# Kernel optimization log

Measured on AMD Instinct MI355X. Metric: run time of the kernel, lower is better.

The kernel has to match this reference:

```python
import jax, jax.numpy as jnp
import numpy as np

B, T, C, IMG = 16, 1024, 4, 64
HID_C = 16                 # self.c (hidden_dim before *image_size)
H = HID_C * IMG            # 1024 GRU hidden size
IN = C * IMG               # 256 GRU input size
L = 2                      # num_layers


def setup_inputs() -> dict:
    key = jax.random.key(0)
    ks = jax.random.split(key, 10)
    s_in = 1.0 / np.sqrt(H)
    return {
        "x": jax.random.normal(ks[0], (B, T, C, IMG), jnp.float32),
        "h0": jnp.zeros((L, B, H), jnp.float32),
        "w_ih_0": jax.random.normal(ks[1], (3 * H, IN), jnp.float32) * s_in,
        "w_hh_0": jax.random.normal(ks[2], (3 * H, H), jnp.float32) * s_in,
        "b_ih_0": jax.random.normal(ks[3], (3 * H,), jnp.float32) * s_in,
        "b_hh_0": jax.random.normal(ks[4], (3 * H,), jnp.float32) * s_in,
        "w_ih_1": jax.random.normal(ks[5], (3 * H, H), jnp.float32) * s_in,
        "w_hh_1": jax.random.normal(ks[6], (3 * H, H), jnp.float32) * s_in,
        "b_ih_1": jax.random.normal(ks[7], (3 * H,), jnp.float32) * s_in,
        "b_hh_1": jax.random.normal(ks[8], (3 * H,), jnp.float32) * s_in,
    }


def _gru_layer(xs, h0, w_ih, w_hh, b_ih, b_hh):
    # xs: [b,t,in], h0: [b,H]. Precompute input-gate matmuls over all t.
    gx = jnp.einsum("bti,gi->btg", xs, w_ih) + b_ih  # [b,t,3H]

    def step(hprev, gx_t):
        gh = hprev @ w_hh.T + b_hh                   # [b,3H]
        xr, xz, xn = jnp.split(gx_t, 3, axis=-1)
        hr, hz, hn = jnp.split(gh, 3, axis=-1)
        r = jax.nn.sigmoid(xr + hr)
        z = jax.nn.sigmoid(xz + hz)
        n = jnp.tanh(xn + r * hn)
        hnew = (1.0 - z) * n + z * hprev
        return hnew, hnew

    h_last, ys = jax.lax.scan(step, h0, jnp.swapaxes(gx, 0, 1))
    return jnp.swapaxes(ys, 0, 1), h_last            # [b,t,H], [b,H]


def reference(x, h0, w_ih_0, w_hh_0, b_ih_0, b_hh_0,
              w_ih_1, w_hh_1, b_ih_1, b_hh_1):
    b, t, c, h = x.shape
    xs = x.reshape(b, t, c * h)
    y0, h_last0 = _gru_layer(xs, h0[0], w_ih_0, w_hh_0, b_ih_0, b_hh_0)
    y1, h_last1 = _gru_layer(y0, h0[1], w_ih_1, w_hh_1, b_ih_1, b_hh_1)
    y = y1.reshape(b, t, HID_C, h)
    last_states = jnp.stack([h_last0, h_last1], axis=0)  # [L,b,H]
    return y, last_states
```

## Files before the change

### kernel.cpp

```cpp
#include <hip/hip_runtime.h>
#include <stdint.h>

#define T_ 1024

typedef float  floatx4 __attribute__((ext_vector_type(4)));
typedef short  shortx8 __attribute__((ext_vector_type(8)));
typedef unsigned long long u64;

union U16 { u64 q[2]; unsigned d[4]; shortx8 v; };

__device__ __forceinline__ unsigned short f2bf(float f) {
  union { float f; unsigned u; } v; v.f = f;
  return (unsigned short)((v.u + 0x7FFFu + ((v.u >> 16) & 1u)) >> 16);
}
__device__ __forceinline__ unsigned pkbf(float lo, float hi) {
  unsigned r;
  asm("v_cvt_pk_bf16_f32 %0, %1, %2" : "=v"(r) : "v"(lo), "v"(hi));
  return r;
}
__device__ __forceinline__ u64 lda(const u64* p) {
  return __hip_atomic_load(p, __ATOMIC_RELAXED, __HIP_MEMORY_SCOPE_AGENT);
}
__device__ __forceinline__ void sta(u64* p, u64 v) {
  __hip_atomic_store(p, v, __ATOMIC_RELAXED, __HIP_MEMORY_SCOPE_AGENT);
}

__global__ void prep_kernel(uint4* __restrict__ fz) {
  long gid = (long)blockIdx.x * 256 + threadIdx.x;
  if (gid < 786432L) { uint4 z; z.x = z.y = z.z = z.w = 0u; fz[gid] = z; }
}

#define MFMA __builtin_amdgcn_mfma_f32_16x16x32_bf16

template<int L>
__device__ __forceinline__ void gru_wave(int lb, int tid,
    const float* __restrict__ x,
    const float* __restrict__ whh, const float* __restrict__ wih,
    const float* __restrict__ bih, const float* __restrict__ bhh,
    u64* __restrict__ y0buf, u64* __restrict__ h1ring,
    u64* __restrict__ f0, u64* __restrict__ f1,
    float* __restrict__ dout,
    short* __restrict__ wlds, float (*part)[4][4][16][17])
{
  constexpr int KW  = L ? 2048 : 1280;
  constexpr int WS  = KW + 8;
  constexpr int NC  = L ? 8 : 16;
  constexpr int NR  = 3 * NC;
  constexpr int KXs = L ? 1024 : 256;
  const int cb = lb * NC;
  const int w  = tid >> 6;
  const int l  = tid & 63;
  const int lr = l & 15, lq = l >> 4;
  const int c  = L ? (lr & 7) : lr;

  for (int i = tid; i < NR * (KW / 8); i += 256) {
    int row = i / (KW / 8);
    int k   = (i % (KW / 8)) * 8;
    int g = row / NC, cc = row % NC;
    const float* src = (k < 1024) ? (whh + (long)(g * 1024 + cb + cc) * 1024 + k)
                                  : (wih + (long)(g * 1024 + cb + cc) * KXs + (k - 1024));
    float4 a = *(const float4*)src;
    float4 b = *(const float4*)(src + 4);
    uint4 t4;
    t4.x = pkbf(a.x, a.y); t4.y = pkbf(a.z, a.w);
    t4.z = pkbf(b.x, b.y); t4.w = pkbf(b.z, b.w);
    *(uint4*)(wlds + row * WS + k) = t4;
  }

  const int gb = tid >> (L ? 3 : 4);
  const int gc = tid & (NC - 1);
  const bool isg = tid < 16 * NC;
  float bir = 0, biz = 0, bin = 0, bhr = 0, bhz = 0, bhn = 0;
  if (isg) {
    bir = bih[cb + gc];        bhr = bhh[cb + gc];
    biz = bih[1024 + cb + gc]; bhz = bhh[1024 + cb + gc];
    bin = bih[2048 + cb + gc]; bhn = bhh[2048 + cb + gc];
  }
  __syncthreads();

  const short* w0 = wlds + (0 * NC + c) * WS;
  const short* w1 = wlds + (1 * NC + c) * WS;
  const short* w2 = wlds + (2 * NC + c) * WS;

  float hp = 0.f;

  for (int t = 0; t < T_; ++t) {
    floatx4 ar = {0.f, 0.f, 0.f, 0.f};
    floatx4 az = ar, anh = ar, anx = ar;

    if constexpr (L == 0) {
#pragma unroll
      for (int j = 0; j < 2; ++j) {
        const int kt = w * 2 + j;
        const float* xs = x + (long)lr * 262144 + (long)t * 256 + kt * 32 + lq * 8;
        float4 a = *(const float4*)xs;
        float4 b = *(const float4*)(xs + 4);
        U16 u;
        u.d[0] = pkbf(a.x, a.y); u.d[1] = pkbf(a.z, a.w);
        u.d[2] = pkbf(b.x, b.y); u.d[3] = pkbf(b.z, b.w);
        const int ko = 1024 + kt * 32 + lq * 8;
        ar  = MFMA(u.v, *(const shortx8*)(w0 + ko), ar,  0, 0, 0);
        az  = MFMA(u.v, *(const shortx8*)(w1 + ko), az,  0, 0, 0);
        anx = MFMA(u.v, *(const shortx8*)(w2 + ko), anx, 0, 0, 0);
      }
      if (t > 0) {
        const u64* fp = f0 + ((long)(t - 1) * 64 + (w * 16 + lr)) * 8 + lq;
        for (;;) {
          u64 fl = lda(fp);
          if (__all(fl != 0)) break;
          __builtin_amdgcn_s_sleep(1);
        }
        const u64* base = y0buf + ((long)(t - 1) * 16 + lr) * 256 + w * 64 + lq * 2;
        u64 q[16];
#pragma unroll
        for (int j = 0; j < 8; ++j) {
          q[2 * j]     = lda(base + j * 8);
          q[2 * j + 1] = lda(base + j * 8 + 1);
        }
#pragma unroll
        for (int j = 0; j < 8; ++j) {
          U16 u; u.q[0] = q[2 * j]; u.q[1] = q[2 * j + 1];
          const int ko = (w * 8 + j) * 32 + lq * 8;
          ar  = MFMA(u.v, *(const shortx8*)(w0 + ko), ar,  0, 0, 0);
          az  = MFMA(u.v, *(const shortx8*)(w1 + ko), az,  0, 0, 0);
          anh = MFMA(u.v, *(const shortx8*)(w2 + ko), anh, 0, 0, 0);
        }
      }
    } else {
      const u64* fpy = f0 + ((long)t * 64 + (w * 16 + lr)) * 8 + lq;
      const u64* fph = f1 + ((long)(t > 0 ? t - 1 : 0) * 128 + (w * 32 + (l & 31))) * 8 + (l >> 5);
      for (;;) {
        u64 fy = lda(fpy);
        u64 fh = (t > 0) ? lda(fph) : 1ull;
        if (__all(fy != 0 && fh != 0)) break;
        __builtin_amdgcn_s_sleep(1);
      }
      const u64* yb = y0buf + ((long)t * 16 + lr) * 256 + w * 64 + lq * 2;
      u64 qy[16], qh[16];
#pragma unroll
      for (int j = 0; j < 8; ++j) {
        qy[2 * j]     = lda(yb + j * 8);
        qy[2 * j + 1] = lda(yb + j * 8 + 1);
      }
      if (t > 0) {
        const u64* hb = h1ring + ((long)((t - 1) & 7) * 16 + lr) * 256 + w * 64 + lq * 2;
#pragma unroll
        for (int j = 0; j < 8; ++j) {
          qh[2 * j]     = lda(hb + j * 8);
          qh[2 * j + 1] = lda(hb + j * 8 + 1);
        }
      }
#pragma unroll
      for (int j = 0; j < 8; ++j) {
        U16 u; u.q[0] = qy[2 * j]; u.q[1] = qy[2 * j + 1];
        const int ko = 1024 + (w * 8 + j) * 32 + lq * 8;
        ar  = MFMA(u.v, *(const shortx8*)(w0 + ko), ar,  0, 0, 0);
        az  = MFMA(u.v, *(const shortx8*)(w1 + ko), az,  0, 0, 0);
        anx = MFMA(u.v, *(const shortx8*)(w2 + ko), anx, 0, 0, 0);
      }
      if (t > 0) {
#pragma unroll
        for (int j = 0; j < 8; ++j) {
          U16 u; u.q[0] = qh[2 * j]; u.q[1] = qh[2 * j + 1];
          const int ko = (w * 8 + j) * 32 + lq * 8;
          ar  = MFMA(u.v, *(const shortx8*)(w0 + ko), ar,  0, 0, 0);
          az  = MFMA(u.v, *(const shortx8*)(w1 + ko), az,  0, 0, 0);
          anh = MFMA(u.v, *(const shortx8*)(w2 + ko), anh, 0, 0, 0);
        }
      }
    }

    const int par = t & 1;
    if (L == 0 || lr < 8) {
#pragma unroll
      for (int r4 = 0; r4 < 4; ++r4) {
        const int b = lq * 4 + r4;
        part[par][w][0][b][lr] = ar[r4];
        part[par][w][1][b][lr] = az[r4];
        part[par][w][2][b][lr] = anh[r4];
        part[par][w][3][b][lr] = anx[r4];
      }
    }
    __syncthreads();

    if (isg) {
      float sr = 0, sz = 0, snh = 0, snx = 0;
#pragma unroll
      for (int ww = 0; ww < 4; ++ww) {
        sr  += part[par][ww][0][gb][gc];
        sz  += part[par][ww][1][gb][gc];
        snh += part[par][ww][2][gb][gc];
        snx += part[par][ww][3][gb][gc];
      }
      float r = 1.f / (1.f + __expf(-(sr + bir + bhr)));
      float z = 1.f / (1.f + __expf(-(sz + biz + bhz)));
      float targ = snx + bin + r * (snh + bhn);
      float e2 = __expf(2.f * targ);
      float n = 1.f - 2.f / (e2 + 1.f);
      float hn = (1.f - z) * n + z * hp;
      hp = hn;

      unsigned hv = f2bf(hn);
      unsigned v1 = (unsigned)__shfl_down((int)hv, 1);
      unsigned v2 = (unsigned)__shfl_down((int)hv, 2);
      unsigned v3 = (unsigned)__shfl_down((int)hv, 3);

      if constexpr (L == 0) {
        if ((gc & 3) == 0) {
          u64 word = (u64)(hv | (v1 << 16)) | ((u64)(v2 | (v3 << 16)) << 32);
          sta(y0buf + ((long)t * 16 + gb) * 256 + ((cb + gc) >> 2), word);
        }
        asm volatile("s_waitcnt vmcnt(0)" ::: "memory");
        if (l == 0)
          sta(f0 + ((long)t * 64 + lb) * 8 + w, 1ull);
        if (t == T_ - 1)
          dout[16777216L + (long)gb * 1024 + cb + gc] = hn;
      } else {
        if ((gc & 3) == 0) {
          u64 word = (u64)(hv | (v1 << 16)) | ((u64)(v2 | (v3 << 16)) << 32);
          sta(h1ring + ((long)(t & 7) * 16 + gb) * 256 + ((cb + gc) >> 2), word);
        }
        asm volatile("s_waitcnt vmcnt(0)" ::: "memory");
        if (l == 0)
          sta(f1 + ((long)t * 128 + lb) * 8 + w, 1ull);
        unsigned fv = __float_as_uint(hn);
        unsigned fw2 = (unsigned)__shfl_down((int)fv, 1);
        if ((gc & 1) == 0)
          *(u64*)(dout + (long)gb * 1048576 + (long)t * 1024 + cb + gc) =
              (u64)fv | ((u64)fw2 << 32);
        if (t == T_ - 1)
          dout[16777216L + 16384 + (long)gb * 1024 + cb + gc] = hn;
      }
    }
  }
}

__global__ __launch_bounds__(256, 1) void gru_kernel(
    const float* __restrict__ x,
    const float* __restrict__ whh0, const float* __restrict__ wih0,
    const float* __restrict__ bih0, const float* __restrict__ bhh0,
    const float* __restrict__ whh1, const float* __restrict__ wih1,
    const float* __restrict__ bih1, const float* __restrict__ bhh1,
    u64* y0buf, u64* h1ring, u64* f0, u64* f1, float* dout)
{
  __shared__ __align__(16) short wlds[48 * 1288];
  __shared__ float part[2][4][4][16][17];
  const int bid = blockIdx.x, tid = threadIdx.x;
  if (bid < 64)
    gru_wave<0>(bid, tid, x, whh0, wih0, bih0, bhh0, y0buf, h1ring, f0, f1, dout, wlds, part);
  else
    gru_wave<1>(bid - 64, tid, x, whh1, wih1, bih1, bhh1, y0buf, h1ring, f0, f1, dout, wlds, part);
}

extern "C" void kernel_launch(void* const* d_in, const int* in_sizes, int n_in,
                              void* d_out, int out_size, void* d_ws, size_t ws_size,
                              hipStream_t stream) {
  (void)in_sizes; (void)n_in; (void)out_size; (void)ws_size;
  const float* x    = (const float*)d_in[0];
  const float* wih0 = (const float*)d_in[2];
  const float* whh0 = (const float*)d_in[3];
  const float* bih0 = (const float*)d_in[4];
  const float* bhh0 = (const float*)d_in[5];
  const float* wih1 = (const float*)d_in[6];
  const float* whh1 = (const float*)d_in[7];
  const float* bih1 = (const float*)d_in[8];
  const float* bhh1 = (const float*)d_in[9];
  char* ws = (char*)d_ws;
  u64* y0buf  = (u64*)(ws + 0L);
  u64* h1ring = (u64*)(ws + 33554432L);
  u64* f0     = (u64*)(ws + 33816576L);
  u64* f1     = (u64*)(ws + 38010880L);
  float* out  = (float*)d_out;

  prep_kernel<<<3072, 256, 0, stream>>>((uint4*)f0);
  gru_kernel<<<192, 256, 0, stream>>>(x, whh0, wih0, bih0, bhh0,
                                      whh1, wih1, bih1, bhh1,
                                      y0buf, h1ring, f0, f1, out);
}
```

Baseline: 6.362 ms.

## Use one flag per block instead of per-wave flags for cross-block step signaling

```diff
diff --git a/kernel.cpp b/kernel.cpp
--- a/kernel.cpp
+++ b/kernel.cpp
@@ -27,7 +27,7 @@
 
 __global__ void prep_kernel(uint4* __restrict__ fz) {
   long gid = (long)blockIdx.x * 256 + threadIdx.x;
-  if (gid < 786432L) { uint4 z; z.x = z.y = z.z = z.w = 0u; fz[gid] = z; }
+  if (gid < 98304L) { uint4 z; z.x = z.y = z.z = z.w = 0u; fz[gid] = z; }
 }
 
 #define MFMA __builtin_amdgcn_mfma_f32_16x16x32_bf16
@@ -104,7 +104,7 @@
         anx = MFMA(u.v, *(const shortx8*)(w2 + ko), anx, 0, 0, 0);
       }
       if (t > 0) {
-        const u64* fp = f0 + ((long)(t - 1) * 64 + (w * 16 + lr)) * 8 + lq;
+        const u64* fp = f0 + (long)(t - 1) * 64 + l;
         for (;;) {
           u64 fl = lda(fp);
           if (__all(fl != 0)) break;
@@ -127,13 +127,13 @@
         }
       }
     } else {
-      const u64* fpy = f0 + ((long)t * 64 + (w * 16 + lr)) * 8 + lq;
-      const u64* fph = f1 + ((long)(t > 0 ? t - 1 : 0) * 128 + (w * 32 + (l & 31))) * 8 + (l >> 5);
-      for (;;) {
-        u64 fy = lda(fpy);
-        u64 fh = (t > 0) ? lda(fph) : 1ull;
-        if (__all(fy != 0 && fh != 0)) break;
-        __builtin_amdgcn_s_sleep(1);
+      {
+        const u64* fy = f0 + (long)t * 64 + l;
+        for (;;) {
+          u64 fl = lda(fy);
+          if (__all(fl != 0)) break;
+          __builtin_amdgcn_s_sleep(1);
+        }
       }
       const u64* yb = y0buf + ((long)t * 16 + lr) * 256 + w * 64 + lq * 2;
       u64 qy[16], qh[16];
@@ -143,6 +143,12 @@
         qy[2 * j + 1] = lda(yb + j * 8 + 1);
       }
       if (t > 0) {
+        const u64* fh = f1 + (long)(t - 1) * 128 + l;
+        for (;;) {
+          u64 a = lda(fh), b = lda(fh + 64);
+          if (__all(a != 0 && b != 0)) break;
+          __builtin_amdgcn_s_sleep(1);
+        }
         const u64* hb = h1ring + ((long)((t - 1) & 7) * 16 + lr) * 256 + w * 64 + lq * 2;
 #pragma unroll
         for (int j = 0; j < 8; ++j) {
@@ -183,6 +189,7 @@
     }
     __syncthreads();
 
+    float hn = 0.f;
     if (isg) {
       float sr = 0, sz = 0, snh = 0, snx = 0;
 #pragma unroll
@@ -197,39 +204,39 @@
       float targ = snx + bin + r * (snh + bhn);
       float e2 = __expf(2.f * targ);
       float n = 1.f - 2.f / (e2 + 1.f);
-      float hn = (1.f - z) * n + z * hp;
+      hn = (1.f - z) * n + z * hp;
       hp = hn;
 
       unsigned hv = f2bf(hn);
       unsigned v1 = (unsigned)__shfl_down((int)hv, 1);
       unsigned v2 = (unsigned)__shfl_down((int)hv, 2);
       unsigned v3 = (unsigned)__shfl_down((int)hv, 3);
-
-      if constexpr (L == 0) {
-        if ((gc & 3) == 0) {
-          u64 word = (u64)(hv | (v1 << 16)) | ((u64)(v2 | (v3 << 16)) << 32);
+      if ((gc & 3) == 0) {
+        u64 word = (u64)(hv | (v1 << 16)) | ((u64)(v2 | (v3 << 16)) << 32);
+        if constexpr (L == 0)
           sta(y0buf + ((long)t * 16 + gb) * 256 + ((cb + gc) >> 2), word);
-        }
-        asm volatile("s_waitcnt vmcnt(0)" ::: "memory");
-        if (l == 0)
-          sta(f0 + ((long)t * 64 + lb) * 8 + w, 1ull);
+        else
+          sta(h1ring + ((long)(t & 7) * 16 + gb) * 256 + ((cb + gc) >> 2), word);
+      }
+    }
+
+    asm volatile("s_waitcnt vmcnt(0)" ::: "memory");
+    __syncthreads();
+    if (tid == 0)
+      sta((L ? f1 + (long)t * 128 : f0 + (long)t * 64) + lb, 1ull);
+
+    if (isg) {
+      if constexpr (L == 1) {
+        unsigned fv = __float_as_uint(hn);
+        unsigned f2v = (unsigned)__shfl_down((int)fv, 1);
+        if ((gc & 1) == 0)
+          *(u64*)(dout + (long)gb * 1048576 + (long)t * 1024 + cb + gc) =
+              (u64)fv | ((u64)f2v << 32);
+        if (t == T_ - 1)
+          dout[16777216L + 16384 + (long)gb * 1024 + cb + gc] = hn;
+      } else {
         if (t == T_ - 1)
           dout[16777216L + (long)gb * 1024 + cb + gc] = hn;
-      } else {
-        if ((gc & 3) == 0) {
-          u64 word = (u64)(hv | (v1 << 16)) | ((u64)(v2 | (v3 << 16)) << 32);
-          sta(h1ring + ((long)(t & 7) * 16 + gb) * 256 + ((cb + gc) >> 2), word);
-        }
-        asm volatile("s_waitcnt vmcnt(0)" ::: "memory");
-        if (l == 0)
-          sta(f1 + ((long)t * 128 + lb) * 8 + w, 1ull);
-        unsigned fv = __float_as_uint(hn);
-        unsigned fw2 = (unsigned)__shfl_down((int)fv, 1);
-        if ((gc & 1) == 0)
-          *(u64*)(dout + (long)gb * 1048576 + (long)t * 1024 + cb + gc) =
-              (u64)fv | ((u64)fw2 << 32);
-        if (t == T_ - 1)
-          dout[16777216L + 16384 + (long)gb * 1024 + cb + gc] = hn;
       }
     }
   }
@@ -269,10 +276,10 @@
   u64* y0buf  = (u64*)(ws + 0L);
   u64* h1ring = (u64*)(ws + 33554432L);
   u64* f0     = (u64*)(ws + 33816576L);
-  u64* f1     = (u64*)(ws + 38010880L);
+  u64* f1     = (u64*)(ws + 34340864L);
   float* out  = (float*)d_out;
 
-  prep_kernel<<<3072, 256, 0, stream>>>((uint4*)f0);
+  prep_kernel<<<384, 256, 0, stream>>>((uint4*)f0);
   gru_kernel<<<192, 256, 0, stream>>>(x, whh0, wih0, bih0, bhh0,
                                       whh1, wih1, bih1, bhh1,
                                       y0buf, h1ring, f0, f1, out);
```

New measurement: 5.766 ms. 9.4% less time.
